# Kernel optimization log

Hardware: AMD Instinct MI355X
Metric: run time of the kernel (lower is better)

## Reference

```python
import jax, jax.numpy as jnp
import numpy as np

EPS = 1e-5

def _ada_ln(x, c, W_ss, b_ss):
    # LayerNorm without affine, then conditional scale/bias from c via SiLU->Linear
    mu = jnp.mean(x, axis=-1, keepdims=True)
    var = jnp.mean((x - mu) ** 2, axis=-1, keepdims=True)
    h = (x - mu) / jnp.sqrt(var + EPS)
    ss = jax.nn.silu(c) @ W_ss + b_ss            # [B, 2H]
    scale, bias = jnp.split(ss, 2, axis=-1)      # [B, H] each
    return (1.0 + scale)[:, None, :] * h + bias[:, None, :]

def setup_inputs() -> dict:
    key = jax.random.key(0)
    ks = jax.random.split(key, 12)
    B, Lq, Lkv, H = 8, 2048, 512, 1024
    s = 0.02
    return {
        "x_q": jax.random.normal(ks[0], (B, Lq, H), jnp.float32),
        "x_kv": jax.random.normal(ks[1], (B, Lkv, H), jnp.float32),
        "t_vec": jax.random.normal(ks[2], (B, H), jnp.float32),
        "Wq": jax.random.normal(ks[3], (H, H), jnp.float32) * s,
        "bq": jnp.zeros((H,), jnp.float32),
        "Wkv": jax.random.normal(ks[4], (H, 2 * H), jnp.float32) * s,
        "bkv": jnp.zeros((2 * H,), jnp.float32),
        "Wp": jax.random.normal(ks[5], (H, H), jnp.float32) * s,
        "bp": jnp.zeros((H,), jnp.float32),
        "Wss_q": jax.random.normal(ks[6], (H, 2 * H), jnp.float32) * s,
        "bss_q": jnp.zeros((2 * H,), jnp.float32),
        "Wss_kv": jax.random.normal(ks[7], (H, 2 * H), jnp.float32) * s,
        "bss_kv": jnp.zeros((2 * H,), jnp.float32),
    }

def reference(x_q, x_kv, t_vec, Wq, bq, Wkv, bkv, Wp, bp, Wss_q, bss_q, Wss_kv, bss_kv):
    B, Lq, H = x_q.shape
    Lkv = x_kv.shape[1]
    nh = 16
    dh = H // nh

    xq = _ada_ln(x_q, t_vec, Wss_q, bss_q)
    xkv = _ada_ln(x_kv, t_vec, Wss_kv, bss_kv)

    q = (xq @ Wq + bq).reshape(B, Lq, nh, dh)          # [B,Lq,h,d]
    kv = (xkv @ Wkv + bkv).reshape(B, Lkv, 2, nh, dh)
    k = kv[:, :, 0]                                     # [B,Lkv,h,d]
    v = kv[:, :, 1]

    scores = jnp.einsum("bqhd,bkhd->bhqk", q, k) / jnp.sqrt(jnp.float32(dh))
    attn = jax.nn.softmax(scores, axis=-1)
    out = jnp.einsum("bhqk,bkhd->bqhd", attn, v).reshape(B, Lq, H)
    return x_q + (out @ Wp + bp)
```

## Files before the change

kernel.cpp:

```cpp
#include <hip/hip_runtime.h>
#include <hip/hip_bf16.h>
#include <stdint.h>

typedef __attribute__((ext_vector_type(8))) short bf16x8;
typedef __attribute__((ext_vector_type(4))) float f32x4;
typedef __attribute__((ext_vector_type(4))) _Float16 f16x4;
typedef __attribute__((ext_vector_type(8))) _Float16 f16x8;
typedef __attribute__((ext_vector_type(4))) unsigned short u16x4;

__device__ __forceinline__ float b2f(unsigned short u){
  union { unsigned int i; float f; } x; x.i = ((unsigned int)u) << 16; return x.f;
}
__device__ __forceinline__ unsigned short f2b(float f){
  union { float f; unsigned int i; } x; x.f = f;
  unsigned int r = x.i + 0x7fffu + ((x.i >> 16) & 1u);
  return (unsigned short)(r >> 16);
}

__device__ __forceinline__ void gld_lds16(const void* g, void* l){
  __builtin_amdgcn_global_load_lds((const __attribute__((address_space(1))) unsigned int*)g,
                                   (__attribute__((address_space(3))) unsigned int*)l,
                                   16, 0, 0);
}

__global__ __launch_bounds__(256) void transpose_k(const float* __restrict__ in,
                                                   unsigned short* __restrict__ out,
                                                   int R, int C){
  __shared__ unsigned short tile[32][33];
  int tx = threadIdx.x & 31, ty = threadIdx.x >> 5;
  int r0 = blockIdx.y * 32, c0 = blockIdx.x * 32;
#pragma unroll
  for (int t = 0; t < 4; ++t)
    tile[ty + t*8][tx] = f2b(in[(size_t)(r0 + ty + t*8) * C + c0 + tx]);
  __syncthreads();
#pragma unroll
  for (int t = 0; t < 4; ++t)
    out[(size_t)(c0 + ty + t*8) * R + r0 + tx] = tile[tx][ty + t*8];
}

__global__ __launch_bounds__(256) void ss_init_k(const float* __restrict__ bssq,
                                                 const float* __restrict__ bssk,
                                                 float* __restrict__ ss_q,
                                                 float* __restrict__ ss_kv){
  int idx = blockIdx.x*256 + threadIdx.x;
  int which = idx >> 14, rem = idx & 16383;
  int j = rem & 2047;
  if (which) ss_kv[rem] = bssk[j];
  else       ss_q[rem]  = bssq[j];
}

__global__ __launch_bounds__(256) void ss2_k(const float* __restrict__ tvec,
                                             const float* __restrict__ Wssq,
                                             const float* __restrict__ Wssk,
                                             float* __restrict__ ss_q,
                                             float* __restrict__ ss_kv){
  const int which = blockIdx.z;
  const float* W = which ? Wssk : Wssq;
  float* ss = which ? ss_kv : ss_q;
  const int col = blockIdx.x*256 + threadIdx.x;
  const int k0 = blockIdx.y*64;

  __shared__ float sl[8][64];
  int idx = threadIdx.x;
#pragma unroll
  for (int t = 0; t < 2; ++t){
    int i = idx + t*256;
    int b = i >> 6, k = i & 63;
    float c = tvec[b*1024 + k0 + k];
    sl[b][k] = c / (1.f + __expf(-c));
  }
  __syncthreads();

  float acc[8] = {0.f,0.f,0.f,0.f,0.f,0.f,0.f,0.f};
#pragma unroll 8
  for (int k = 0; k < 64; ++k){
    float w = W[(size_t)(k0 + k)*2048 + col];
#pragma unroll
    for (int b = 0; b < 8; ++b) acc[b] += sl[b][k] * w;
  }
#pragma unroll
  for (int b = 0; b < 8; ++b)
    atomicAdd(&ss[b*2048 + col], acc[b]);
}

__global__ __launch_bounds__(256) void ada_ln_k(const float* __restrict__ x,
                                                const float* __restrict__ ss,
                                                unsigned short* __restrict__ out,
                                                int L){
  int row = blockIdx.x;
  int b = row / L;
  const float* xr = x + (size_t)row * 1024;
  int tid = threadIdx.x;
  float4 v = *(const float4*)&xr[tid*4];
  float s = v.x + v.y + v.z + v.w;
  __shared__ float red[4];
#pragma unroll
  for (int o = 32; o > 0; o >>= 1) s += __shfl_xor(s, o, 64);
  if ((tid & 63) == 0) red[tid >> 6] = s;
  __syncthreads();
  float mu = (red[0]+red[1]+red[2]+red[3]) * (1.f/1024.f);
  __syncthreads();
  float vs = (v.x-mu)*(v.x-mu) + (v.y-mu)*(v.y-mu) + (v.z-mu)*(v.z-mu) + (v.w-mu)*(v.w-mu);
#pragma unroll
  for (int o = 32; o > 0; o >>= 1) vs += __shfl_xor(vs, o, 64);
  if ((tid & 63) == 0) red[tid >> 6] = vs;
  __syncthreads();
  float var = (red[0]+red[1]+red[2]+red[3]) * (1.f/1024.f);
  float inv = rsqrtf(var + 1e-5f);
  const float* sb = ss + (size_t)b*2048;
  float4 sc = *(const float4*)&sb[tid*4];
  float4 bi = *(const float4*)&sb[1024 + tid*4];
  u16x4 o4;
  o4[0] = f2b((1.f + sc.x) * ((v.x-mu)*inv) + bi.x);
  o4[1] = f2b((1.f + sc.y) * ((v.y-mu)*inv) + bi.y);
  o4[2] = f2b((1.f + sc.z) * ((v.z-mu)*inv) + bi.z);
  o4[3] = f2b((1.f + sc.w) * ((v.w-mu)*inv) + bi.w);
  *(u16x4*)&out[(size_t)row*1024 + tid*4] = o4;
}

__global__ __launch_bounds__(256) void gemm_bt_k(const unsigned short* __restrict__ A,
                                                 const unsigned short* __restrict__ BT,
                                                 const float* __restrict__ bias,
                                                 const float* __restrict__ resf,
                                                 unsigned short* __restrict__ Cb,
                                                 float* __restrict__ Cf,
                                                 _Float16* __restrict__ vT,
                                                 int M, int N, int K, int mode){
  __shared__ __attribute__((aligned(16))) unsigned short As[2][128*64];
  __shared__ __attribute__((aligned(16))) unsigned short Bs[2][128*64];
  const int tid = threadIdx.x;
  const int wave = tid >> 6, lane = tid & 63;
  const int lm = lane & 15, quad = lane >> 4;

  const int gx = gridDim.x;
  const int nwg = gx * gridDim.y;
  const int lid = blockIdx.y * gx + blockIdx.x;
  const int chunk = nwg >> 3;
  const int tile = (lid & 7) * chunk + (lid >> 3);
  const int m0 = (tile / gx) * 128, n0 = (tile % gx) * 128;

  const int wm = (wave >> 1) * 64, wn = (wave & 1) * 64;
  f32x4 acc[4][4];
#pragma unroll
  for (int i = 0; i < 4; ++i)
#pragma unroll
    for (int j = 0; j < 4; ++j) acc[i][j] = (f32x4){0.f,0.f,0.f,0.f};

  int rowc[4], colc[4];
#pragma unroll
  for (int r = 0; r < 4; ++r){
    int c = r*256 + tid;
    rowc[r] = c >> 3; colc[r] = (c & 7) * 8;
  }

#define STAGE128(buf, kk)                                                              \
  {                                                                                    \
    _Pragma("unroll")                                                                  \
    for (int r = 0; r < 4; ++r)                                                        \
      gld_lds16(&A[(size_t)(m0 + rowc[r])*K + (kk) + colc[r]], &As[buf][(r*256 + tid)*8]); \
    _Pragma("unroll")                                                                  \
    for (int r = 0; r < 4; ++r)                                                        \
      gld_lds16(&BT[(size_t)(n0 + rowc[r])*K + (kk) + colc[r]], &Bs[buf][(r*256 + tid)*8]); \
  }

  const int NT = K >> 6;
  STAGE128(0, 0);
  __syncthreads();

  int cur = 0;
  for (int t = 0; t < NT; ++t){
    if (t + 1 < NT) STAGE128(cur ^ 1, (t + 1) << 6);
#pragma unroll
    for (int ks = 0; ks < 2; ++ks){
      bf16x8 af[4], bfr[4];
#pragma unroll
      for (int i = 0; i < 4; ++i)
        af[i] = *(bf16x8*)&As[cur][(wm + i*16 + lm)*64 + ks*32 + quad*8];
#pragma unroll
      for (int j = 0; j < 4; ++j)
        bfr[j] = *(bf16x8*)&Bs[cur][(wn + j*16 + lm)*64 + ks*32 + quad*8];
#pragma unroll
      for (int i = 0; i < 4; ++i)
#pragma unroll
        for (int j = 0; j < 4; ++j)
          acc[i][j] = __builtin_amdgcn_mfma_f32_16x16x32_bf16(af[i], bfr[j], acc[i][j], 0, 0, 0);
    }
    __syncthreads();
    cur ^= 1;
  }
#undef STAGE128

  if (mode == 2 && n0 >= 1024){
#pragma unroll
    for (int j = 0; j < 4; ++j){
      int col = n0 + wn + j*16 + lm;
      int d = col - 1024;
      float bv = bias[col];
#pragma unroll
      for (int i = 0; i < 4; ++i){
        int rowb = m0 + wm + i*16 + quad*4;
        int brow = rowb >> 9, l = rowb & 511;
        f16x4 h4;
#pragma unroll
        for (int p = 0; p < 4; ++p) h4[p] = (_Float16)(acc[i][j][p] + bv);
        *(f16x4*)&vT[((size_t)brow*1024 + d)*512 + l] = h4;
      }
    }
    return;
  }

#pragma unroll
  for (int j = 0; j < 4; ++j){
    int col = n0 + wn + j*16 + lm;
    float bv = bias[col];
#pragma unroll
    for (int i = 0; i < 4; ++i){
#pragma unroll
      for (int p = 0; p < 4; ++p){
        int row = m0 + wm + i*16 + quad*4 + p;
        float v = acc[i][j][p] + bv;
        if (mode == 1){
          Cf[(size_t)row*N + col] = v + resf[(size_t)row*N + col];
        } else {
          Cb[(size_t)row*1024 + col] = f2b(v);
        }
      }
    }
  }
}

__global__ __launch_bounds__(512) void gemm256_k(const unsigned short* __restrict__ A,
                                                 const unsigned short* __restrict__ BT,
                                                 const float* __restrict__ bias,
                                                 const float* __restrict__ resf,
                                                 unsigned short* __restrict__ Cb,
                                                 float* __restrict__ Cf,
                                                 int M, int N, int K, int mode){
  __shared__ __attribute__((aligned(16))) unsigned short As[2][256*64];
  __shared__ __attribute__((aligned(16))) unsigned short Bs[2][256*64];
  const int tid = threadIdx.x;
  const int wave = tid >> 6, lane = tid & 63;
  const int lm = lane & 15, quad = lane >> 4;

  const int gx = gridDim.x;
  const int nwg = gx * gridDim.y;
  const int lid = blockIdx.y * gx + blockIdx.x;
  const int chunk = nwg >> 3;
  const int tile = (lid & 7) * chunk + (lid >> 3);
  const int m0 = (tile / gx) * 256, n0 = (tile % gx) * 256;

  const int wm = (wave >> 2) * 128, wn = (wave & 3) * 64;

  f32x4 acc[8][4];
#pragma unroll
  for (int i = 0; i < 8; ++i)
#pragma unroll
    for (int j = 0; j < 4; ++j) acc[i][j] = (f32x4){0.f,0.f,0.f,0.f};

  int rowc[4], colc[4];
#pragma unroll
  for (int r = 0; r < 4; ++r){
    int c = r*512 + tid;
    rowc[r] = c >> 3; colc[r] = (c & 7) * 8;
  }

#define STAGE256(buf, kk)                                                              \
  {                                                                                    \
    _Pragma("unroll")                                                                  \
    for (int r = 0; r < 4; ++r)                                                        \
      gld_lds16(&A[(size_t)(m0 + rowc[r])*K + (kk) + colc[r]], &As[buf][(r*512 + tid)*8]); \
    _Pragma("unroll")                                                                  \
    for (int r = 0; r < 4; ++r)                                                        \
      gld_lds16(&BT[(size_t)(n0 + rowc[r])*K + (kk) + colc[r]], &Bs[buf][(r*512 + tid)*8]); \
  }

  const int NT = K >> 6;
  STAGE256(0, 0);
  __syncthreads();

  int cur = 0;
  for (int t = 0; t < NT; ++t){
    if (t + 1 < NT) STAGE256(cur ^ 1, (t + 1) << 6);
#pragma unroll
    for (int ks = 0; ks < 2; ++ks){
      bf16x8 af[8], bfr[4];
#pragma unroll
      for (int i = 0; i < 8; ++i)
        af[i] = *(bf16x8*)&As[cur][(wm + i*16 + lm)*64 + ks*32 + quad*8];
#pragma unroll
      for (int j = 0; j < 4; ++j)
        bfr[j] = *(bf16x8*)&Bs[cur][(wn + j*16 + lm)*64 + ks*32 + quad*8];
#pragma unroll
      for (int i = 0; i < 8; ++i)
#pragma unroll
        for (int j = 0; j < 4; ++j)
          acc[i][j] = __builtin_amdgcn_mfma_f32_16x16x32_bf16(af[i], bfr[j], acc[i][j], 0, 0, 0);
    }
    __syncthreads();
    cur ^= 1;
  }
#undef STAGE256

#pragma unroll
  for (int j = 0; j < 4; ++j){
    int col = n0 + wn + j*16 + lm;
    float bv = bias[col];
#pragma unroll
    for (int i = 0; i < 8; ++i){
#pragma unroll
      for (int p = 0; p < 4; ++p){
        int row = m0 + wm + i*16 + quad*4 + p;
        float v = acc[i][j][p] + bv;
        if (mode == 1){
          Cf[(size_t)row*N + col] = v + resf[(size_t)row*N + col];
        } else {
          Cb[(size_t)row*1024 + col] = f2b(v);
        }
      }
    }
  }
}

__global__ __launch_bounds__(256) void attn_k(const unsigned short* __restrict__ q,
                                              const unsigned short* __restrict__ kbuf,
                                              const _Float16* __restrict__ vT,
                                              unsigned short* __restrict__ out){
  const int lid = (blockIdx.z * gridDim.y + blockIdx.y) * gridDim.x + blockIdx.x;
  const int tile = (lid & 7) * 256 + (lid >> 3);
  const int qb = tile & 15, h = (tile >> 4) & 15, b = tile >> 8;
  const int tid = threadIdx.x;
  const int wave = tid >> 6, lane = tid & 63;
  const int lm = lane & 15, quad = lane >> 4;
  const int q0 = qb * 128;

  __shared__ __attribute__((aligned(16))) unsigned short Ks[64*72];
  __shared__ __attribute__((aligned(16))) _Float16      Vs[64*72];

  bf16x8 qf[2][2];
#pragma unroll
  for (int u = 0; u < 2; ++u){
    const unsigned short* qrow = q + ((size_t)b*2048 + q0 + wave*32 + u*16 + lm)*1024 + h*64;
    qf[u][0] = *(const bf16x8*)&qrow[quad*8];
    qf[u][1] = *(const bf16x8*)&qrow[32 + quad*8];
  }

  const unsigned short* kb = kbuf + ((size_t)b*512)*1024 + h*64;
  const _Float16*       vb = vT + ((size_t)b*1024 + h*64)*512;

  f32x4 oacc[2][4];
#pragma unroll
  for (int u = 0; u < 2; ++u)
#pragma unroll
    for (int nt = 0; nt < 4; ++nt) oacc[u][nt] = (f32x4){0.f,0.f,0.f,0.f};
  float m_run[2] = {-1e30f, -1e30f}, l_run[2] = {0.f, 0.f};

  const int srow = tid >> 3, scol = (tid & 7) * 8;

  for (int kt = 0; kt < 8; ++kt){
    const int l0 = kt * 64;
    __syncthreads();
#pragma unroll
    for (int r = 0; r < 2; ++r){
      int row = r*32 + srow;
      *(bf16x8*)&Ks[row*72 + scol] = *(const bf16x8*)&kb[(size_t)(l0 + row)*1024 + scol];
      *(f16x8*)&Vs[row*72 + scol]  = *(const f16x8*)&vb[(size_t)row*512 + l0 + scol];
    }
    __syncthreads();

    f32x4 sacc[2][4];
#pragma unroll
    for (int u = 0; u < 2; ++u)
#pragma unroll
      for (int s = 0; s < 4; ++s) sacc[u][s] = (f32x4){0.f,0.f,0.f,0.f};
#pragma unroll
    for (int s = 0; s < 4; ++s){
      bf16x8 kf0 = *(bf16x8*)&Ks[(s*16 + lm)*72 + quad*8];
      bf16x8 kf1 = *(bf16x8*)&Ks[(s*16 + lm)*72 + 32 + quad*8];
#pragma unroll
      for (int u = 0; u < 2; ++u){
        sacc[u][s] = __builtin_amdgcn_mfma_f32_16x16x32_bf16(kf0, qf[u][0], sacc[u][s], 0, 0, 0);
        sacc[u][s] = __builtin_amdgcn_mfma_f32_16x16x32_bf16(kf1, qf[u][1], sacc[u][s], 0, 0, 0);
      }
    }

    f16x4 pf[2][4];
#pragma unroll
    for (int u = 0; u < 2; ++u){
      float tm = -1e30f;
#pragma unroll
      for (int s = 0; s < 4; ++s)
#pragma unroll
        for (int p = 0; p < 4; ++p) tm = fmaxf(tm, sacc[u][s][p]);
      tm = fmaxf(tm, __shfl_xor(tm, 16, 64));
      tm = fmaxf(tm, __shfl_xor(tm, 32, 64));
      float m_new = fmaxf(m_run[u], tm * 0.125f);
      float alpha = __expf(m_run[u] - m_new);
      m_run[u] = m_new;
      l_run[u] *= alpha;
      float ap[4];
#pragma unroll
      for (int p = 0; p < 4; ++p) ap[p] = __shfl(alpha, quad*4 + p, 64);
#pragma unroll
      for (int nt = 0; nt < 4; ++nt){
        oacc[u][nt][0] *= ap[0]; oacc[u][nt][1] *= ap[1];
        oacc[u][nt][2] *= ap[2]; oacc[u][nt][3] *= ap[3];
      }
#pragma unroll
      for (int s = 0; s < 4; ++s)
#pragma unroll
        for (int p = 0; p < 4; ++p){
          float e = __expf(sacc[u][s][p] * 0.125f - m_new);
          l_run[u] += e;
          pf[u][s][p] = (_Float16)e;
        }
    }

#pragma unroll
    for (int s = 0; s < 4; ++s){
#pragma unroll
      for (int nt = 0; nt < 4; ++nt){
        f16x4 vf = *(const f16x4*)&Vs[(size_t)(nt*16 + lm)*72 + s*16 + quad*4];
#pragma unroll
        for (int u = 0; u < 2; ++u)
          oacc[u][nt] = __builtin_amdgcn_mfma_f32_16x16x16f16(pf[u][s], vf, oacc[u][nt], 0, 0, 0);
      }
    }
  }

#pragma unroll
  for (int u = 0; u < 2; ++u){
    float lr = l_run[u];
    lr += __shfl_xor(lr, 16, 64);
    lr += __shfl_xor(lr, 32, 64);
    float rinv = 1.f / lr;
    float rp[4];
#pragma unroll
    for (int p = 0; p < 4; ++p) rp[p] = __shfl(rinv, quad*4 + p, 64);
    const size_t obase = ((size_t)b*2048 + q0 + wave*32 + u*16) * 1024 + h*64;
#pragma unroll
    for (int nt = 0; nt < 4; ++nt)
#pragma unroll
      for (int p = 0; p < 4; ++p){
        int row = quad*4 + p;
        out[obase + (size_t)row*1024 + nt*16 + lm] = f2b(oacc[u][nt][p] * rp[p]);
      }
  }
}

extern "C" void kernel_launch(void* const* d_in, const int* in_sizes, int n_in,
                              void* d_out, int out_size, void* d_ws, size_t ws_size,
                              hipStream_t stream){
  const float* x_q  = (const float*)d_in[0];
  const float* x_kv = (const float*)d_in[1];
  const float* tvec = (const float*)d_in[2];
  const float* Wq   = (const float*)d_in[3];
  const float* bq   = (const float*)d_in[4];
  const float* Wkv  = (const float*)d_in[5];
  const float* bkv  = (const float*)d_in[6];
  const float* Wp   = (const float*)d_in[7];
  const float* bp   = (const float*)d_in[8];
  const float* Wssq = (const float*)d_in[9];
  const float* bssq = (const float*)d_in[10];
  const float* Wssk = (const float*)d_in[11];
  const float* bssk = (const float*)d_in[12];

  char* ws = (char*)d_ws;
  float*          ss_q  = (float*)(ws + 0);
  float*          ss_kv = (float*)(ws + 65536);
  unsigned short* xq    = (unsigned short*)(ws + 131072);
  unsigned short* xkv   = (unsigned short*)(ws + 33685504);
  unsigned short* qbuf  = (unsigned short*)(ws + 42074112);
  unsigned short* kbuf  = (unsigned short*)(ws + 75628544);
  _Float16*       vTbuf = (_Float16*)     (ws + 84017152);
  unsigned short* WqT   = (unsigned short*)(ws + 92405760);
  unsigned short* WkvT  = (unsigned short*)(ws + 94502912);
  unsigned short* WpT   = (unsigned short*)(ws + 98697216);

  dim3 blk(256);
  transpose_k<<<dim3(32, 32), blk, 0, stream>>>(Wq,  WqT,  1024, 1024);
  transpose_k<<<dim3(64, 32), blk, 0, stream>>>(Wkv, WkvT, 1024, 2048);
  transpose_k<<<dim3(32, 32), blk, 0, stream>>>(Wp,  WpT,  1024, 1024);

  ss_init_k<<<dim3(128), blk, 0, stream>>>(bssq, bssk, ss_q, ss_kv);
  ss2_k<<<dim3(8, 16, 2), blk, 0, stream>>>(tvec, Wssq, Wssk, ss_q, ss_kv);

  ada_ln_k<<<dim3(16384), blk, 0, stream>>>(x_q,  ss_q,  xq,  2048);
  ada_ln_k<<<dim3(4096),  blk, 0, stream>>>(x_kv, ss_kv, xkv, 512);

  gemm256_k<<<dim3(4, 64), dim3(512), 0, stream>>>(xq, WqT, bq, nullptr, qbuf, nullptr,
                                                   16384, 1024, 1024, 0);
  gemm_bt_k<<<dim3(16, 32), blk, 0, stream>>>(xkv, WkvT, bkv, nullptr, kbuf, nullptr, vTbuf,
                                              4096, 2048, 1024, 2);

  attn_k<<<dim3(16, 16, 8), blk, 0, stream>>>(qbuf, kbuf, vTbuf, xq);

  gemm256_k<<<dim3(4, 64), dim3(512), 0, stream>>>(xq, WpT, bp, x_q, nullptr, (float*)d_out,
                                                   16384, 1024, 1024, 1);
}
```

Baseline: 433.6 us.

## Prefetch two K-tiles ahead with vmcnt waits and XOR-swizzle LDS in 256 GEMM

Both GEMM kernels now issue loads for the first two K-tiles up front. Each step waits with s_waitcnt vmcnt(8) only for the older tile, so one tile of global-to-LDS traffic stays in flight while the MFMAs run. Full __syncthreads is replaced by raw s_barrier pairs. The 256x256 kernel also XOR-swizzles the source column of each staged 16-byte chunk and the matching LDS read offset, to reduce LDS bank conflicts on fragment reads. The explicit waitcnt handling is fragile: the counts must match exactly 8 loads per stage, and the compiler may insert other memory ops.

```diff
diff --git a/kernel.cpp b/kernel.cpp
--- a/kernel.cpp
+++ b/kernel.cpp
@@ -165,11 +165,12 @@
 
   const int NT = K >> 6;
   STAGE128(0, 0);
-  __syncthreads();
-
-  int cur = 0;
+  STAGE128(1, 64);
+  asm volatile("s_waitcnt vmcnt(8)" ::: "memory");
+  __builtin_amdgcn_s_barrier();
+
   for (int t = 0; t < NT; ++t){
-    if (t + 1 < NT) STAGE128(cur ^ 1, (t + 1) << 6);
+    const int cur = t & 1;
 #pragma unroll
     for (int ks = 0; ks < 2; ++ks){
       bf16x8 af[4], bfr[4];
@@ -185,8 +186,16 @@
         for (int j = 0; j < 4; ++j)
           acc[i][j] = __builtin_amdgcn_mfma_f32_16x16x32_bf16(af[i], bfr[j], acc[i][j], 0, 0, 0);
     }
-    __syncthreads();
-    cur ^= 1;
+    if (t + 1 < NT){
+      __builtin_amdgcn_s_barrier();
+      if (t + 2 < NT){
+        STAGE128(cur, (t + 2) << 6);
+        asm volatile("s_waitcnt vmcnt(8)" ::: "memory");
+      } else {
+        asm volatile("s_waitcnt vmcnt(0)" ::: "memory");
+      }
+      __builtin_amdgcn_s_barrier();
+    }
   }
 #undef STAGE128
 
@@ -257,47 +266,59 @@
 #pragma unroll
     for (int j = 0; j < 4; ++j) acc[i][j] = (f32x4){0.f,0.f,0.f,0.f};
 
-  int rowc[4], colc[4];
+  int rowc[4], colsw[4];
 #pragma unroll
   for (int r = 0; r < 4; ++r){
     int c = r*512 + tid;
-    rowc[r] = c >> 3; colc[r] = (c & 7) * 8;
+    rowc[r]  = c >> 3;
+    colsw[r] = ((c & 7) ^ (rowc[r] & 7)) * 8;
   }
 
 #define STAGE256(buf, kk)                                                              \
   {                                                                                    \
     _Pragma("unroll")                                                                  \
     for (int r = 0; r < 4; ++r)                                                        \
-      gld_lds16(&A[(size_t)(m0 + rowc[r])*K + (kk) + colc[r]], &As[buf][(r*512 + tid)*8]); \
+      gld_lds16(&A[(size_t)(m0 + rowc[r])*K + (kk) + colsw[r]], &As[buf][(r*512 + tid)*8]); \
     _Pragma("unroll")                                                                  \
     for (int r = 0; r < 4; ++r)                                                        \
-      gld_lds16(&BT[(size_t)(n0 + rowc[r])*K + (kk) + colc[r]], &Bs[buf][(r*512 + tid)*8]); \
+      gld_lds16(&BT[(size_t)(n0 + rowc[r])*K + (kk) + colsw[r]], &Bs[buf][(r*512 + tid)*8]); \
   }
 
   const int NT = K >> 6;
   STAGE256(0, 0);
-  __syncthreads();
-
-  int cur = 0;
+  STAGE256(1, 64);
+  asm volatile("s_waitcnt vmcnt(8)" ::: "memory");
+  __builtin_amdgcn_s_barrier();
+
+  const int rsw = lm & 7;
   for (int t = 0; t < NT; ++t){
-    if (t + 1 < NT) STAGE256(cur ^ 1, (t + 1) << 6);
+    const int cur = t & 1;
 #pragma unroll
     for (int ks = 0; ks < 2; ++ks){
+      const int rc = ((ks*4 + quad) ^ rsw) * 8;
       bf16x8 af[8], bfr[4];
 #pragma unroll
       for (int i = 0; i < 8; ++i)
-        af[i] = *(bf16x8*)&As[cur][(wm + i*16 + lm)*64 + ks*32 + quad*8];
+        af[i] = *(bf16x8*)&As[cur][(wm + i*16 + lm)*64 + rc];
 #pragma unroll
       for (int j = 0; j < 4; ++j)
-        bfr[j] = *(bf16x8*)&Bs[cur][(wn + j*16 + lm)*64 + ks*32 + quad*8];
+        bfr[j] = *(bf16x8*)&Bs[cur][(wn + j*16 + lm)*64 + rc];
 #pragma unroll
       for (int i = 0; i < 8; ++i)
 #pragma unroll
         for (int j = 0; j < 4; ++j)
           acc[i][j] = __builtin_amdgcn_mfma_f32_16x16x32_bf16(af[i], bfr[j], acc[i][j], 0, 0, 0);
     }
-    __syncthreads();
-    cur ^= 1;
+    if (t + 1 < NT){
+      __builtin_amdgcn_s_barrier();
+      if (t + 2 < NT){
+        STAGE256(cur, (t + 2) << 6);
+        asm volatile("s_waitcnt vmcnt(8)" ::: "memory");
+      } else {
+        asm volatile("s_waitcnt vmcnt(0)" ::: "memory");
+      }
+      __builtin_amdgcn_s_barrier();
+    }
   }
 #undef STAGE256
 
```

Result: faster. 417.4 us (-3.7%).
